# Performance work log

Measured on AMD Instinct MI355X. Metric: run time of the kernel, lower is better.

Reference implementation:

```python
import jax, jax.numpy as jnp
import numpy as np

N_PATHS = 10_000_000
MAX_LEN = 3
N_NODES = 100_000
HIDDEN = 128
HEAD = 1


def setup_inputs() -> dict:
    key = jax.random.key(0)
    k1, k2, k3 = jax.random.split(key, 3)
    # path indices in [-1, N_NODES); -1 marks a padding slot (maps to zero score)
    paths = jax.random.randint(k1, (N_PATHS, MAX_LEN), -1, N_NODES, dtype=jnp.int64)
    node_feature = jax.random.normal(k2, (N_NODES, HIDDEN), dtype=jnp.float32)
    # per-step Linear(hidden, head=1, bias=False) weights, stacked: [MAX_LEN, HEAD, HIDDEN]
    W = jax.random.normal(k3, (MAX_LEN, HEAD, HIDDEN), dtype=jnp.float32) * (1.0 / np.sqrt(HIDDEN))
    return {"paths": paths, "node_feature": node_feature, "W": W}


def reference(paths, node_feature, W):
    # per-step scalar node scores: [n_nodes, L, head]
    proj = jnp.einsum("nd,lod->nlo", node_feature, W)
    valid = paths >= 0                         # [P, L]
    safe = jnp.where(valid, paths, 0)          # clamp -1 -> 0 (masked below)
    L = W.shape[0]
    step = jnp.arange(L)[None, :]              # [1, L]
    gathered = proj[safe, step, :]             # [P, L, head]
    gathered = jnp.where(valid[..., None], gathered, jnp.zeros((), proj.dtype))
    path_length = jnp.clip(valid.sum(axis=-1, keepdims=True), 1)  # [P, 1]
    attn_score = gathered.sum(axis=1) / path_length.astype(proj.dtype)  # [P, head]
    return attn_score
```

## Files before the change

### kernel.cpp

```cpp
#include <hip/hip_runtime.h>

#define HIDDEN       128
#define TPB          1024
#define PPT          8
#define CHUNK_NODES  25600
#define CHUNK_BYTES  (3 * CHUNK_NODES * 2)
#define FILL_UNITS   (CHUNK_BYTES / 1024)

typedef int   v4i __attribute__((ext_vector_type(4)));
typedef float v4f __attribute__((ext_vector_type(4)));
typedef unsigned short u16;
typedef unsigned int   u32;

static __device__ __forceinline__ u16 f32_to_f16_bits(float x) {
    union { _Float16 h; u16 u; } cv;
    cv.h = (_Float16)x;
    return cv.u;
}

static __device__ __forceinline__ void gload_lds16(const void* gp, void* lp) {
    __builtin_amdgcn_global_load_lds(
        (const __attribute__((address_space(1))) unsigned int*)gp,
        (__attribute__((address_space(3))) unsigned int*)lp,
        16, 0, 0);
}

__global__ __launch_bounds__(256) void proj_kernel(
    const float* __restrict__ feat,
    const float* __restrict__ W,
    u16* __restrict__ proj_h,
    int n_nodes)
{
    int gtid = blockIdx.x * blockDim.x + threadIdx.x;
    int node = gtid >> 6;
    int lane = threadIdx.x & 63;
    if (node >= n_nodes) return;

    const float2* f2 = (const float2*)(feat + (size_t)node * HIDDEN);
    const float2* w2 = (const float2*)W;

    float2 f   = f2[lane];
    float2 w0  = w2[lane];
    float2 w1  = w2[64 + lane];
    float2 wv2 = w2[128 + lane];

    float s0 = f.x * w0.x  + f.y * w0.y;
    float s1 = f.x * w1.x  + f.y * w1.y;
    float s2 = f.x * wv2.x + f.y * wv2.y;

    #pragma unroll
    for (int off = 32; off > 0; off >>= 1) {
        s0 += __shfl_xor(s0, off, 64);
        s1 += __shfl_xor(s1, off, 64);
        s2 += __shfl_xor(s2, off, 64);
    }

    if (lane == 0) {
        int c     = node / CHUNK_NODES;
        int local = node - c * CHUNK_NODES;
        u16* base = proj_h + (size_t)c * 3 * CHUNK_NODES + local;
        base[0]               = f32_to_f16_bits(s0);
        base[CHUNK_NODES]     = f32_to_f16_bits(s1);
        base[2 * CHUNK_NODES] = f32_to_f16_bits(s2);
    }
}

__global__ __launch_bounds__(TPB, 4) void score_kernel(
    const int* __restrict__ paths,
    const u16* __restrict__ proj_h,
    float* __restrict__ out,
    int n_threads, int nchunks)
{
    extern __shared__ u16 lds[];
    const int dummy = 3 * CHUNK_NODES;

    int t    = blockIdx.x * TPB + threadIdx.x;
    int tl   = t < n_threads ? t : n_threads - 1;
    int wid  = threadIdx.x >> 6;
    int lane = threadIdx.x & 63;

    int ids[3 * PPT];
    const v4i* p4 = (const v4i*)paths;
    #pragma unroll
    for (int i = 0; i < 6; ++i) {
        v4i v = __builtin_nontemporal_load(p4 + (size_t)tl * 6 + i);
        ids[4*i+0] = v.x; ids[4*i+1] = v.y; ids[4*i+2] = v.z; ids[4*i+3] = v.w;
    }

    if (threadIdx.x == 0) lds[dummy] = 0;

    float acc[PPT];
    #pragma unroll
    for (int p = 0; p < PPT; ++p) acc[p] = 0.0f;

    const unsigned char* src  = (const unsigned char*)proj_h;
    char*                ldsb = (char*)lds;

    for (int c = 0; c < nchunks; ++c) {
        const unsigned char* gsrc = src + (size_t)c * CHUNK_BYTES;
        for (int j = wid; j < FILL_UNITS; j += TPB / 64)
            gload_lds16(gsrc + j * 1024 + lane * 16, ldsb + j * 1024);
        __syncthreads();

        int cbase = c * CHUNK_NODES;
        #pragma unroll
        for (int p = 0; p < PPT; ++p) {
            #pragma unroll
            for (int l = 0; l < 3; ++l) {
                u32 loc = (u32)(ids[3*p + l] - cbase);
                int off = (loc < (u32)CHUNK_NODES)
                          ? (l * CHUNK_NODES + (int)loc) : dummy;
                union { u16 u; _Float16 h; } cv;
                cv.u = lds[off];
                acc[p] += (float)cv.h;
            }
        }
        if (c + 1 < nchunks) __syncthreads();
    }

    if (t < n_threads) {
        #pragma unroll
        for (int j = 0; j < PPT / 4; ++j) {
            v4f o;
            #pragma unroll
            for (int q = 0; q < 4; ++q) {
                int p = 4*j + q;
                int cnt = (int)(ids[3*p] >= 0) + (int)(ids[3*p+1] >= 0)
                        + (int)(ids[3*p+2] >= 0);
                float inv = (cnt == 3) ? (1.0f/3.0f) : (cnt == 2 ? 0.5f : 1.0f);
                o[q] = acc[p] * inv;
            }
            __builtin_nontemporal_store(o, ((v4f*)out) + (size_t)t * 2 + j);
        }
    }
}

extern "C" void kernel_launch(void* const* d_in, const int* in_sizes, int n_in,
                              void* d_out, int out_size, void* d_ws, size_t ws_size,
                              hipStream_t stream) {
    const int*   paths = (const int*)d_in[0];
    const float* feat  = (const float*)d_in[1];
    const float* W     = (const float*)d_in[2];
    float*       out   = (float*)d_out;

    int n_nodes = in_sizes[1] / HIDDEN;
    int n_paths = in_sizes[0] / 3;
    u16* proj_h = (u16*)d_ws;

    int nchunks = (n_nodes + CHUNK_NODES - 1) / CHUNK_NODES;
    size_t lds_bytes = (size_t)3 * CHUNK_NODES * sizeof(u16) + 4;

    (void)hipFuncSetAttribute((const void*)score_kernel,
            hipFuncAttributeMaxDynamicSharedMemorySize, (int)lds_bytes);
    (void)hipGetLastError();

    {
        int blocks = (n_nodes + 3) / 4;
        proj_kernel<<<blocks, 256, 0, stream>>>(feat, W, proj_h, n_nodes);
    }

    {
        int n_threads = (n_paths + PPT - 1) / PPT;
        int blocks = (n_threads + TPB - 1) / TPB;
        blocks = ((blocks + 255) / 256) * 256;
        score_kernel<<<blocks, TPB, lds_bytes, stream>>>(paths, proj_h, out,
                                                         n_threads, nchunks);
    }
}
```

Baseline: 288.8 us.

## Use per-step planar fp16 score tables and stage one step-half in LDS

The projected fp16 scores are now stored as three planar arrays, one per path step, instead of chunk-interleaved. The score kernel stages half of one step's plane in LDS at a time, six fills in total, and gathers only that step's index for each path. Each thread now handles 20 paths instead of 8, so fewer blocks launch and the full-table L2-to-LDS refill that every block pays is amortised over more paths. The cost is more registers per thread (60 indices plus 20 accumulators), fewer resident blocks to hide latency, and the last fill reading slightly past the end of the table.

New measurement: 357.3 us. 1.24x slower.

```diff
diff --git a/kernel.cpp b/kernel.cpp
--- a/kernel.cpp
+++ b/kernel.cpp
@@ -1,11 +1,12 @@
 #include <hip/hip_runtime.h>
 
-#define HIDDEN       128
-#define TPB          1024
-#define PPT          8
-#define CHUNK_NODES  25600
-#define CHUNK_BYTES  (3 * CHUNK_NODES * 2)
-#define FILL_UNITS   (CHUNK_BYTES / 1024)
+#define HIDDEN   128
+#define TPB      1024
+#define PPT      20
+#define CN       51200
+#define CN2      102400
+#define DUMMY2   102400
+#define UNITS    (CN2 / 1024)
 
 typedef int   v4i __attribute__((ext_vector_type(4)));
 typedef float v4f __attribute__((ext_vector_type(4)));
@@ -56,12 +57,10 @@
     }
 
     if (lane == 0) {
-        int c     = node / CHUNK_NODES;
-        int local = node - c * CHUNK_NODES;
-        u16* base = proj_h + (size_t)c * 3 * CHUNK_NODES + local;
-        base[0]               = f32_to_f16_bits(s0);
-        base[CHUNK_NODES]     = f32_to_f16_bits(s1);
-        base[2 * CHUNK_NODES] = f32_to_f16_bits(s2);
+        u16* base = proj_h + node;
+        base[0]                   = f32_to_f16_bits(s0);
+        base[n_nodes]             = f32_to_f16_bits(s1);
+        base[2 * (size_t)n_nodes] = f32_to_f16_bits(s2);
     }
 }
 
@@ -69,53 +68,57 @@
     const int* __restrict__ paths,
     const u16* __restrict__ proj_h,
     float* __restrict__ out,
-    int n_threads, int nchunks)
+    int n_threads, int n_nodes, int nh)
 {
     extern __shared__ u16 lds[];
-    const int dummy = 3 * CHUNK_NODES;
+    char* ldsb = (char*)lds;
 
     int t    = blockIdx.x * TPB + threadIdx.x;
     int tl   = t < n_threads ? t : n_threads - 1;
     int wid  = threadIdx.x >> 6;
     int lane = threadIdx.x & 63;
 
-    int ids[3 * PPT];
+    int id2[3 * PPT];
     const v4i* p4 = (const v4i*)paths;
     #pragma unroll
-    for (int i = 0; i < 6; ++i) {
-        v4i v = __builtin_nontemporal_load(p4 + (size_t)tl * 6 + i);
-        ids[4*i+0] = v.x; ids[4*i+1] = v.y; ids[4*i+2] = v.z; ids[4*i+3] = v.w;
+    for (int i = 0; i < 3 * PPT / 4; ++i) {
+        v4i v = __builtin_nontemporal_load(p4 + (size_t)tl * (3 * PPT / 4) + i);
+        id2[4*i+0] = v.x << 1; id2[4*i+1] = v.y << 1;
+        id2[4*i+2] = v.z << 1; id2[4*i+3] = v.w << 1;
     }
 
-    if (threadIdx.x == 0) lds[dummy] = 0;
+    if (threadIdx.x == 0) lds[DUMMY2 / 2] = 0;
 
     float acc[PPT];
     #pragma unroll
     for (int p = 0; p < PPT; ++p) acc[p] = 0.0f;
 
-    const unsigned char* src  = (const unsigned char*)proj_h;
-    char*                ldsb = (char*)lds;
+    const unsigned char* tab = (const unsigned char*)proj_h;
+    int plane_b = 2 * n_nodes;
 
-    for (int c = 0; c < nchunks; ++c) {
-        const unsigned char* gsrc = src + (size_t)c * CHUNK_BYTES;
-        for (int j = wid; j < FILL_UNITS; j += TPB / 64)
-            gload_lds16(gsrc + j * 1024 + lane * 16, ldsb + j * 1024);
-        __syncthreads();
+    for (int h = 0; h < nh; ++h) {
+        int cb2   = h * CN2;
+        int rem_b = plane_b - cb2;
+        int units = rem_b >= CN2 ? UNITS : ((rem_b + 1023) >> 10);
 
-        int cbase = c * CHUNK_NODES;
         #pragma unroll
-        for (int p = 0; p < PPT; ++p) {
+        for (int l = 0; l < 3; ++l) {
+            const unsigned char* src = tab + (size_t)l * plane_b + cb2;
+            for (int j = wid; j < units; j += TPB / 64)
+                gload_lds16(src + (size_t)j * 1024 + lane * 16,
+                            ldsb + j * 1024);
+            __syncthreads();
+
             #pragma unroll
-            for (int l = 0; l < 3; ++l) {
-                u32 loc = (u32)(ids[3*p + l] - cbase);
-                int off = (loc < (u32)CHUNK_NODES)
-                          ? (l * CHUNK_NODES + (int)loc) : dummy;
-                union { u16 u; _Float16 h; } cv;
-                cv.u = lds[off];
-                acc[p] += (float)cv.h;
+            for (int p = 0; p < PPT; ++p) {
+                u32 loc2 = (u32)(id2[3*p + l] - cb2);
+                int off  = loc2 < (u32)CN2 ? (int)loc2 : DUMMY2;
+                union { u16 u; _Float16 hh; } cv;
+                cv.u = *(const u16*)(ldsb + off);
+                acc[p] += (float)cv.hh;
             }
+            if (h + 1 < nh || l < 2) __syncthreads();
         }
-        if (c + 1 < nchunks) __syncthreads();
     }
 
     if (t < n_threads) {
@@ -125,12 +128,12 @@
             #pragma unroll
             for (int q = 0; q < 4; ++q) {
                 int p = 4*j + q;
-                int cnt = (int)(ids[3*p] >= 0) + (int)(ids[3*p+1] >= 0)
-                        + (int)(ids[3*p+2] >= 0);
+                int cnt = (int)(id2[3*p] >= 0) + (int)(id2[3*p+1] >= 0)
+                        + (int)(id2[3*p+2] >= 0);
                 float inv = (cnt == 3) ? (1.0f/3.0f) : (cnt == 2 ? 0.5f : 1.0f);
                 o[q] = acc[p] * inv;
             }
-            __builtin_nontemporal_store(o, ((v4f*)out) + (size_t)t * 2 + j);
+            __builtin_nontemporal_store(o, ((v4f*)out) + (size_t)t * (PPT/4) + j);
         }
     }
 }
@@ -147,8 +150,8 @@
     int n_paths = in_sizes[0] / 3;
     u16* proj_h = (u16*)d_ws;
 
-    int nchunks = (n_nodes + CHUNK_NODES - 1) / CHUNK_NODES;
-    size_t lds_bytes = (size_t)3 * CHUNK_NODES * sizeof(u16) + 4;
+    int nh = (n_nodes + CN - 1) / CN;
+    size_t lds_bytes = (size_t)CN2 + 4;
 
     (void)hipFuncSetAttribute((const void*)score_kernel,
             hipFuncAttributeMaxDynamicSharedMemorySize, (int)lds_bytes);
@@ -164,6 +167,6 @@
         int blocks = (n_threads + TPB - 1) / TPB;
         blocks = ((blocks + 255) / 256) * 256;
         score_kernel<<<blocks, TPB, lds_bytes, stream>>>(paths, proj_h, out,
-                                                         n_threads, nchunks);
+                                                         n_threads, n_nodes, nh);
     }
 }
```
